# Kernel optimization log

Measured on AMD Instinct MI355X. Metric: run time of the kernel, lower is better.

The kernel has to match this reference:

```python
import jax, jax.numpy as jnp
import numpy as np

B, T, I, L, D, O = 256, 512, 512, 128, 4, 2
LN_EPS = 1e-5

def setup_inputs() -> dict:
    key = jax.random.key(0)
    ks = jax.random.split(key, 7)
    x = jax.random.normal(ks[0], (B, T, I), jnp.float32)
    # Xavier-ish scaling keeps the recurrence numerically tame
    W_in = jax.random.normal(ks[1], (L, D, I), jnp.float32) * (1.0 / np.sqrt(I))
    W_liquid = jax.random.normal(ks[2], (L, D, L), jnp.float32) * (1.0 / np.sqrt(L))
    W_gate = jax.random.normal(ks[3], (L, D), jnp.float32)
    b_liquid = jnp.zeros((L,), jnp.float32)
    W_out = jax.random.normal(ks[4], (O, L), jnp.float32) * (1.0 / np.sqrt(L))
    b_out = jnp.zeros((O,), jnp.float32)
    ln_w = jnp.ones((L,), jnp.float32)
    ln_b = jnp.zeros((L,), jnp.float32)
    leaky_rate = jnp.asarray(0.3, jnp.float32)
    return {"x": x, "W_in": W_in, "W_liquid": W_liquid, "W_gate": W_gate,
            "b_liquid": b_liquid, "W_out": W_out, "b_out": b_out,
            "ln_w": ln_w, "ln_b": ln_b, "leaky_rate": leaky_rate}

def reference(x, W_in, W_liquid, W_gate, b_liquid, W_out, b_out, ln_w, ln_b, leaky_rate):
    # Liquid dendritic RNN. Dropout is identity (eval mode).
    gate = jax.nn.sigmoid(W_gate)                                   # [L,D]
    # Input branch has no recurrent dependency -> batch it over all timesteps
    in_br = jax.nn.relu(jnp.einsum('ldi,bti->btld', W_in, x))       # [B,T,L,D]
    merged_in = jnp.einsum('btld,ld->btl', in_br, gate)             # [B,T,L]
    alpha = jax.nn.sigmoid(leaky_rate)

    def step(state, m_in_t):                                        # state [B,L]
        rec_br = jax.nn.relu(jnp.einsum('ldh,bh->bld', W_liquid, state))
        merged_rec = jnp.einsum('bld,ld->bl', rec_br, gate)
        li = m_in_t + merged_rec + b_liquid                         # [B,L]
        mu = jnp.mean(li, axis=-1, keepdims=True)
        var = jnp.var(li, axis=-1, keepdims=True)
        li = (li - mu) * jax.lax.rsqrt(var + LN_EPS) * ln_w + ln_b
        new_state = (1.0 - alpha) * state + alpha * jnp.tanh(li)
        return new_state, None

    state0 = jnp.zeros((x.shape[0], W_in.shape[0]), x.dtype)
    final_state, _ = jax.lax.scan(step, state0, jnp.swapaxes(merged_in, 0, 1))
    return final_state @ W_out.T + b_out                            # [B,O]
```

## Files before the change

kernel.cpp:

```cpp
#include <hip/hip_runtime.h>
#include <hip/hip_bf16.h>
#include <stdint.h>


typedef __bf16 bf16x8 __attribute__((ext_vector_type(8)));
typedef float f32x4_t __attribute__((ext_vector_type(4)));

__device__ inline unsigned short f2bf(float f) {
    union { float f; unsigned u; } v; v.f = f;
    unsigned r = v.u + 0x7fffu + ((v.u >> 16) & 1u);
    return (unsigned short)(r >> 16);
}

__global__ __launch_bounds__(256, 2)
void gemm_in_kernel(const float* __restrict__ x, const float* __restrict__ W_in,
                    const float* __restrict__ W_gate, float* __restrict__ merged)
{
    __shared__ unsigned short As[128 * 32];
    __shared__ unsigned short Bs[128 * 32];

    const int tid = threadIdx.x;
    const int m0 = blockIdx.y * 128;
    const int n0 = blockIdx.x * 128;
    const int lane = tid & 63;
    const int wid  = tid >> 6;
    const int wr = wid >> 1, wc = wid & 1;
    const int fr = lane & 15, fq = lane >> 4;

    f32x4_t acc[4][4];
    #pragma unroll
    for (int i = 0; i < 4; ++i)
        #pragma unroll
        for (int j = 0; j < 4; ++j)
            acc[i][j] = (f32x4_t){0.f, 0.f, 0.f, 0.f};

    for (int k0 = 0; k0 < 512; k0 += 32) {
        #pragma unroll
        for (int p = 0; p < 4; ++p) {
            int ch = tid + p * 256;
            int r  = ch >> 3;
            int c  = ch & 7;
            float4 va = *(const float4*)(x    + (size_t)(m0 + r) * 512 + k0 + c * 4);
            float4 vb = *(const float4*)(W_in + (size_t)(n0 + r) * 512 + k0 + c * 4);
            ushort4 ha, hb;
            ha.x = f2bf(va.x); ha.y = f2bf(va.y); ha.z = f2bf(va.z); ha.w = f2bf(va.w);
            hb.x = f2bf(vb.x); hb.y = f2bf(vb.y); hb.z = f2bf(vb.z); hb.w = f2bf(vb.w);
            *(ushort4*)(&As[r * 32 + c * 4]) = ha;
            *(ushort4*)(&Bs[r * 32 + c * 4]) = hb;
        }
        __syncthreads();

        bf16x8 af[4], bfr[4];
        #pragma unroll
        for (int mi = 0; mi < 4; ++mi)
            af[mi] = *(const bf16x8*)(&As[(wr * 64 + mi * 16 + fr) * 32 + fq * 8]);
        #pragma unroll
        for (int ni = 0; ni < 4; ++ni)
            bfr[ni] = *(const bf16x8*)(&Bs[(wc * 64 + ni * 16 + fr) * 32 + fq * 8]);

        #pragma unroll
        for (int mi = 0; mi < 4; ++mi)
            #pragma unroll
            for (int ni = 0; ni < 4; ++ni)
                acc[mi][ni] = __builtin_amdgcn_mfma_f32_16x16x32_bf16(
                                  af[mi], bfr[ni], acc[mi][ni], 0, 0, 0);
        __syncthreads();
    }

    float gv[4];
    #pragma unroll
    for (int ni = 0; ni < 4; ++ni) {
        int n = n0 + wc * 64 + ni * 16 + fr;
        gv[ni] = 1.f / (1.f + __expf(-W_gate[n]));
    }
    #pragma unroll
    for (int mi = 0; mi < 4; ++mi) {
        #pragma unroll
        for (int ni = 0; ni < 4; ++ni) {
            int n = n0 + wc * 64 + ni * 16 + fr;
            int l = n >> 2;
            #pragma unroll
            for (int j = 0; j < 4; ++j) {
                float v = acc[mi][ni][j];
                float r = fmaxf(v, 0.f) * gv[ni];
                r += __shfl_xor(r, 1);
                r += __shfl_xor(r, 2);
                if ((lane & 3) == 0) {
                    int row = m0 + wr * 64 + mi * 16 + fq * 4 + j;
                    merged[(size_t)row * 128 + l] = r;
                }
            }
        }
    }
}

__global__ __launch_bounds__(512, 2)
void scan_kernel(const float* __restrict__ merged, const float* __restrict__ W_liq,
                 const float* __restrict__ W_gate, const float* __restrict__ b_liq,
                 const float* __restrict__ W_out, const float* __restrict__ b_out,
                 const float* __restrict__ ln_w, const float* __restrict__ ln_b,
                 const float* __restrict__ leaky, float* __restrict__ out)
{
    __shared__ __align__(16) unsigned short s_bf[128];
    __shared__ __align__(16) float red[16];
    __shared__ float s_final[128];

    const int tid  = threadIdx.x;
    const int b    = blockIdx.x;
    const int lane = tid & 63;
    const int w    = tid >> 6;
    const int fr   = lane & 15;
    const int fq   = lane >> 4;

    bf16x8 wfrag[4][4];
    #pragma unroll
    for (int mi = 0; mi < 4; ++mi) {
        const float* wrow = W_liq + (size_t)(w * 64 + mi * 16 + fr) * 128;
        #pragma unroll
        for (int kk = 0; kk < 4; ++kk) {
            float4 f0 = *(const float4*)(wrow + kk * 32 + fq * 8);
            float4 f1 = *(const float4*)(wrow + kk * 32 + fq * 8 + 4);
            union { unsigned short u[8]; bf16x8 v; } cv;
            cv.u[0] = f2bf(f0.x); cv.u[1] = f2bf(f0.y);
            cv.u[2] = f2bf(f0.z); cv.u[3] = f2bf(f0.w);
            cv.u[4] = f2bf(f1.x); cv.u[5] = f2bf(f1.y);
            cv.u[6] = f2bf(f1.z); cv.u[7] = f2bf(f1.w);
            wfrag[mi][kk] = cv.v;
        }
    }

    int   l_mi[4];
    float gv[4][4], blv[4], lwv[4], lbv[4];
    size_t midx[4];
    #pragma unroll
    for (int mi = 0; mi < 4; ++mi) {
        int l = w * 16 + mi * 4 + fq;
        l_mi[mi] = l;
        #pragma unroll
        for (int r = 0; r < 4; ++r)
            gv[mi][r] = 1.f / (1.f + __expf(-W_gate[l * 4 + r]));
        blv[mi] = b_liq[l];
        lwv[mi] = ln_w[l];
        lbv[mi] = ln_b[l];
        midx[mi] = (size_t)b * 65536 + l;
    }
    const float alpha = 1.f / (1.f + __expf(-leaky[0]));
    const float oma   = 1.f - alpha;

    float s_reg[4] = {0.f, 0.f, 0.f, 0.f};
    float cur[4];
    #pragma unroll
    for (int mi = 0; mi < 4; ++mi) cur[mi] = merged[midx[mi]];

    if (tid < 64) ((unsigned*)s_bf)[tid] = 0u;
    __syncthreads();

    const f32x4_t z = {0.f, 0.f, 0.f, 0.f};

    for (int t = 0; t < 512; ++t) {
        bf16x8 bfr[4];
        #pragma unroll
        for (int kk = 0; kk < 4; ++kk)
            bfr[kk] = *(const bf16x8*)(&s_bf[kk * 32 + fq * 8]);

        float nxt[4] = {0.f, 0.f, 0.f, 0.f};
        if (t < 511) {
            #pragma unroll
            for (int mi = 0; mi < 4; ++mi)
                nxt[mi] = merged[midx[mi] + (size_t)(t + 1) * 128];
        }

        f32x4_t acc[4];
        #pragma unroll
        for (int mi = 0; mi < 4; ++mi)
            acc[mi] = __builtin_amdgcn_mfma_f32_16x16x32_bf16(wfrag[mi][0], bfr[0], z, 0, 0, 0);
        #pragma unroll
        for (int kk = 1; kk < 4; ++kk)
            #pragma unroll
            for (int mi = 0; mi < 4; ++mi)
                acc[mi] = __builtin_amdgcn_mfma_f32_16x16x32_bf16(wfrag[mi][kk], bfr[kk], acc[mi], 0, 0, 0);

        float li[4], v1 = 0.f, v2 = 0.f;
        #pragma unroll
        for (int mi = 0; mi < 4; ++mi) {
            float mr = gv[mi][0] * fmaxf(acc[mi][0], 0.f);
            mr = fmaf(gv[mi][1], fmaxf(acc[mi][1], 0.f), mr);
            mr = fmaf(gv[mi][2], fmaxf(acc[mi][2], 0.f), mr);
            mr = fmaf(gv[mi][3], fmaxf(acc[mi][3], 0.f), mr);
            li[mi] = cur[mi] + mr + blv[mi];
            v1 += li[mi];
            v2 = fmaf(li[mi], li[mi], v2);
        }
        v1 += __shfl_xor(v1, 16);  v2 += __shfl_xor(v2, 16);
        v1 += __shfl_xor(v1, 32);  v2 += __shfl_xor(v2, 32);
        if (lane == 0) { red[w] = v1; red[8 + w] = v2; }
        __syncthreads();

        float4 ra = *(const float4*)&red[0], rb = *(const float4*)&red[4];
        float4 rc = *(const float4*)&red[8], rd = *(const float4*)&red[12];
        float S1 = ((ra.x + ra.y) + (ra.z + ra.w)) + ((rb.x + rb.y) + (rb.z + rb.w));
        float S2 = ((rc.x + rc.y) + (rc.z + rc.w)) + ((rd.x + rd.y) + (rd.z + rd.w));
        float mean = S1 * (1.f / 128.f);
        float var  = fmaf(-mean, mean, S2 * (1.f / 128.f));
        float rstd = rsqrtf(var + 1e-5f);

        #pragma unroll
        for (int mi = 0; mi < 4; ++mi) {
            float t1 = rstd * lwv[mi];
            float xn = fmaf(li[mi], t1, fmaf(-mean, t1, lbv[mi]));
            float e  = __expf(2.f * xn);
            float th = fmaf(-2.f, __builtin_amdgcn_rcpf(e + 1.f), 1.f);
            float ns = fmaf(oma, s_reg[mi], alpha * th);
            s_reg[mi] = ns;
            cur[mi]   = nxt[mi];
        }
        if (fr == 0) {
            #pragma unroll
            for (int mi = 0; mi < 4; ++mi)
                s_bf[l_mi[mi]] = f2bf(s_reg[mi]);
        }
        __syncthreads();
    }

    if (fr == 0) {
        #pragma unroll
        for (int mi = 0; mi < 4; ++mi) s_final[l_mi[mi]] = s_reg[mi];
    }
    __syncthreads();
    if (tid < 2) {
        float accO = b_out[tid];
        #pragma unroll
        for (int h = 0; h < 128; ++h)
            accO = fmaf(s_final[h], W_out[tid * 128 + h], accO);
        out[b * 2 + tid] = accO;
    }
}

extern "C" void kernel_launch(void* const* d_in, const int* in_sizes, int n_in,
                              void* d_out, int out_size, void* d_ws, size_t ws_size,
                              hipStream_t stream)
{
    const float* x      = (const float*)d_in[0];
    const float* W_in   = (const float*)d_in[1];
    const float* W_liq  = (const float*)d_in[2];
    const float* W_gate = (const float*)d_in[3];
    const float* b_liq  = (const float*)d_in[4];
    const float* W_out  = (const float*)d_in[5];
    const float* b_out  = (const float*)d_in[6];
    const float* ln_w   = (const float*)d_in[7];
    const float* ln_b   = (const float*)d_in[8];
    const float* leaky  = (const float*)d_in[9];
    float* out    = (float*)d_out;
    float* merged = (float*)d_ws;

    gemm_in_kernel<<<dim3(4, 1024), 256, 0, stream>>>(x, W_in, W_gate, merged);
    scan_kernel<<<256, 512, 0, stream>>>(merged, W_liq, W_gate, b_liq,
                                         W_out, b_out, ln_w, ln_b, leaky, out);
}
```

Measured before the change: 690.5 us.

## Transpose merged input to time-major, vectorize scan loads, split MFMA chains, lighter barriers

The GEMM kernel now writes the merged input as [B][L][T], so each scan thread can fetch four consecutive timesteps with one float4 load, double-buffered two chunks ahead. The scan loop is unrolled in groups of four steps, and the K=128 MFMA accumulation is split into two independent chains that are summed at the end, shortening the serial dependency. __syncthreads is replaced with an explicit lgkmcnt wait plus s_barrier. The trade-off is a strided, uncoalesced store pattern in the GEMM epilogue, and the hand-written barrier relies on the compiler not reordering global memory accesses around it.

```diff
diff --git a/kernel.cpp b/kernel.cpp
--- a/kernel.cpp
+++ b/kernel.cpp
@@ -12,9 +12,14 @@
     return (unsigned short)(r >> 16);
 }
 
+__device__ inline void lds_barrier() {
+    asm volatile("s_waitcnt lgkmcnt(0)" ::: "memory");
+    __builtin_amdgcn_s_barrier();
+}
+
 __global__ __launch_bounds__(256, 2)
 void gemm_in_kernel(const float* __restrict__ x, const float* __restrict__ W_in,
-                    const float* __restrict__ W_gate, float* __restrict__ merged)
+                    const float* __restrict__ W_gate, float* __restrict__ mt)
 {
     __shared__ unsigned short As[128 * 32];
     __shared__ unsigned short Bs[128 * 32];
@@ -87,7 +92,9 @@
                 r += __shfl_xor(r, 2);
                 if ((lane & 3) == 0) {
                     int row = m0 + wr * 64 + mi * 16 + fq * 4 + j;
-                    merged[(size_t)row * 128 + l] = r;
+                    int bb = row >> 9;
+                    int tt = row & 511;
+                    mt[(size_t)bb * 65536 + (size_t)l * 512 + tt] = r;
                 }
             }
         }
@@ -95,7 +102,7 @@
 }
 
 __global__ __launch_bounds__(512, 2)
-void scan_kernel(const float* __restrict__ merged, const float* __restrict__ W_liq,
+void scan_kernel(const float* __restrict__ mt, const float* __restrict__ W_liq,
                  const float* __restrict__ W_gate, const float* __restrict__ b_liq,
                  const float* __restrict__ W_out, const float* __restrict__ b_out,
                  const float* __restrict__ ln_w, const float* __restrict__ ln_b,
@@ -142,84 +149,98 @@
         blv[mi] = b_liq[l];
         lwv[mi] = ln_w[l];
         lbv[mi] = ln_b[l];
-        midx[mi] = (size_t)b * 65536 + l;
+        midx[mi] = (size_t)b * 65536 + (size_t)l * 512;
     }
     const float alpha = 1.f / (1.f + __expf(-leaky[0]));
     const float oma   = 1.f - alpha;
 
     float s_reg[4] = {0.f, 0.f, 0.f, 0.f};
-    float cur[4];
-    #pragma unroll
-    for (int mi = 0; mi < 4; ++mi) cur[mi] = merged[midx[mi]];
+
+    float4 cur4[4], nxt4[4];
+    #pragma unroll
+    for (int mi = 0; mi < 4; ++mi) cur4[mi] = *(const float4*)(mt + midx[mi]);
+    #pragma unroll
+    for (int mi = 0; mi < 4; ++mi) nxt4[mi] = *(const float4*)(mt + midx[mi] + 4);
 
     if (tid < 64) ((unsigned*)s_bf)[tid] = 0u;
-    __syncthreads();
+    lds_barrier();
 
     const f32x4_t z = {0.f, 0.f, 0.f, 0.f};
 
-    for (int t = 0; t < 512; ++t) {
-        bf16x8 bfr[4];
-        #pragma unroll
-        for (int kk = 0; kk < 4; ++kk)
-            bfr[kk] = *(const bf16x8*)(&s_bf[kk * 32 + fq * 8]);
-
-        float nxt[4] = {0.f, 0.f, 0.f, 0.f};
-        if (t < 511) {
+    for (int ts = 0; ts < 512; ts += 4) {
+        float4 ld4[4];
+        if (ts < 504) {
             #pragma unroll
             for (int mi = 0; mi < 4; ++mi)
-                nxt[mi] = merged[midx[mi] + (size_t)(t + 1) * 128];
-        }
-
-        f32x4_t acc[4];
-        #pragma unroll
-        for (int mi = 0; mi < 4; ++mi)
-            acc[mi] = __builtin_amdgcn_mfma_f32_16x16x32_bf16(wfrag[mi][0], bfr[0], z, 0, 0, 0);
-        #pragma unroll
-        for (int kk = 1; kk < 4; ++kk)
-            #pragma unroll
-            for (int mi = 0; mi < 4; ++mi)
-                acc[mi] = __builtin_amdgcn_mfma_f32_16x16x32_bf16(wfrag[mi][kk], bfr[kk], acc[mi], 0, 0, 0);
-
-        float li[4], v1 = 0.f, v2 = 0.f;
-        #pragma unroll
-        for (int mi = 0; mi < 4; ++mi) {
-            float mr = gv[mi][0] * fmaxf(acc[mi][0], 0.f);
-            mr = fmaf(gv[mi][1], fmaxf(acc[mi][1], 0.f), mr);
-            mr = fmaf(gv[mi][2], fmaxf(acc[mi][2], 0.f), mr);
-            mr = fmaf(gv[mi][3], fmaxf(acc[mi][3], 0.f), mr);
-            li[mi] = cur[mi] + mr + blv[mi];
-            v1 += li[mi];
-            v2 = fmaf(li[mi], li[mi], v2);
-        }
-        v1 += __shfl_xor(v1, 16);  v2 += __shfl_xor(v2, 16);
-        v1 += __shfl_xor(v1, 32);  v2 += __shfl_xor(v2, 32);
-        if (lane == 0) { red[w] = v1; red[8 + w] = v2; }
-        __syncthreads();
-
-        float4 ra = *(const float4*)&red[0], rb = *(const float4*)&red[4];
-        float4 rc = *(const float4*)&red[8], rd = *(const float4*)&red[12];
-        float S1 = ((ra.x + ra.y) + (ra.z + ra.w)) + ((rb.x + rb.y) + (rb.z + rb.w));
-        float S2 = ((rc.x + rc.y) + (rc.z + rc.w)) + ((rd.x + rd.y) + (rd.z + rd.w));
-        float mean = S1 * (1.f / 128.f);
-        float var  = fmaf(-mean, mean, S2 * (1.f / 128.f));
-        float rstd = rsqrtf(var + 1e-5f);
-
-        #pragma unroll
-        for (int mi = 0; mi < 4; ++mi) {
-            float t1 = rstd * lwv[mi];
-            float xn = fmaf(li[mi], t1, fmaf(-mean, t1, lbv[mi]));
-            float e  = __expf(2.f * xn);
-            float th = fmaf(-2.f, __builtin_amdgcn_rcpf(e + 1.f), 1.f);
-            float ns = fmaf(oma, s_reg[mi], alpha * th);
-            s_reg[mi] = ns;
-            cur[mi]   = nxt[mi];
-        }
-        if (fr == 0) {
-            #pragma unroll
-            for (int mi = 0; mi < 4; ++mi)
-                s_bf[l_mi[mi]] = f2bf(s_reg[mi]);
-        }
-        __syncthreads();
+                ld4[mi] = *(const float4*)(mt + midx[mi] + ts + 8);
+        }
+
+        #pragma unroll
+        for (int ph = 0; ph < 4; ++ph) {
+            bf16x8 bfr[4];
+            #pragma unroll
+            for (int kk = 0; kk < 4; ++kk)
+                bfr[kk] = *(const bf16x8*)(&s_bf[kk * 32 + fq * 8]);
+
+            f32x4_t a0[4], a1[4];
+            #pragma unroll
+            for (int mi = 0; mi < 4; ++mi) {
+                a0[mi] = __builtin_amdgcn_mfma_f32_16x16x32_bf16(wfrag[mi][0], bfr[0], z, 0, 0, 0);
+                a1[mi] = __builtin_amdgcn_mfma_f32_16x16x32_bf16(wfrag[mi][2], bfr[2], z, 0, 0, 0);
+            }
+            #pragma unroll
+            for (int mi = 0; mi < 4; ++mi) {
+                a0[mi] = __builtin_amdgcn_mfma_f32_16x16x32_bf16(wfrag[mi][1], bfr[1], a0[mi], 0, 0, 0);
+                a1[mi] = __builtin_amdgcn_mfma_f32_16x16x32_bf16(wfrag[mi][3], bfr[3], a1[mi], 0, 0, 0);
+            }
+
+            float li[4], v1 = 0.f, v2 = 0.f;
+            #pragma unroll
+            for (int mi = 0; mi < 4; ++mi) {
+                f32x4_t s4 = a0[mi] + a1[mi];
+                float mr = gv[mi][0] * fmaxf(s4[0], 0.f);
+                mr = fmaf(gv[mi][1], fmaxf(s4[1], 0.f), mr);
+                mr = fmaf(gv[mi][2], fmaxf(s4[2], 0.f), mr);
+                mr = fmaf(gv[mi][3], fmaxf(s4[3], 0.f), mr);
+                li[mi] = cur4[mi][ph] + mr + blv[mi];
+                v1 += li[mi];
+                v2 = fmaf(li[mi], li[mi], v2);
+            }
+            v1 += __shfl_xor(v1, 16);  v2 += __shfl_xor(v2, 16);
+            v1 += __shfl_xor(v1, 32);  v2 += __shfl_xor(v2, 32);
+            if (lane == 0) { red[w] = v1; red[8 + w] = v2; }
+            lds_barrier();
+
+            float4 ra = *(const float4*)&red[0], rb = *(const float4*)&red[4];
+            float4 rc = *(const float4*)&red[8], rd = *(const float4*)&red[12];
+            float S1 = ((ra.x + ra.y) + (ra.z + ra.w)) + ((rb.x + rb.y) + (rb.z + rb.w));
+            float S2 = ((rc.x + rc.y) + (rc.z + rc.w)) + ((rd.x + rd.y) + (rd.z + rd.w));
+            float mean = S1 * (1.f / 128.f);
+            float var  = fmaf(-mean, mean, S2 * (1.f / 128.f));
+            float rstd = rsqrtf(var + 1e-5f);
+
+            #pragma unroll
+            for (int mi = 0; mi < 4; ++mi) {
+                float t1 = rstd * lwv[mi];
+                float xn = fmaf(li[mi], t1, fmaf(-mean, t1, lbv[mi]));
+                float e  = __expf(2.f * xn);
+                float th = fmaf(-2.f, __builtin_amdgcn_rcpf(e + 1.f), 1.f);
+                s_reg[mi] = fmaf(oma, s_reg[mi], alpha * th);
+            }
+            if (fr == 0) {
+                #pragma unroll
+                for (int mi = 0; mi < 4; ++mi)
+                    s_bf[l_mi[mi]] = f2bf(s_reg[mi]);
+            }
+            lds_barrier();
+        }
+
+        #pragma unroll
+        for (int mi = 0; mi < 4; ++mi) cur4[mi] = nxt4[mi];
+        if (ts < 504) {
+            #pragma unroll
+            for (int mi = 0; mi < 4; ++mi) nxt4[mi] = ld4[mi];
+        }
     }
 
     if (fr == 0) {
@@ -250,10 +271,10 @@
     const float* ln_w   = (const float*)d_in[7];
     const float* ln_b   = (const float*)d_in[8];
     const float* leaky  = (const float*)d_in[9];
-    float* out    = (float*)d_out;
-    float* merged = (float*)d_ws;
-
-    gemm_in_kernel<<<dim3(4, 1024), 256, 0, stream>>>(x, W_in, W_gate, merged);
-    scan_kernel<<<256, 512, 0, stream>>>(merged, W_liq, W_gate, b_liq,
+    float* out = (float*)d_out;
+    float* mt  = (float*)d_ws;
+
+    gemm_in_kernel<<<dim3(4, 1024), 256, 0, stream>>>(x, W_in, W_gate, mt);
+    scan_kernel<<<256, 512, 0, stream>>>(mt, W_liq, W_gate, b_liq,
                                          W_out, b_out, ln_w, ln_b, leaky, out);
 }
```

After: 703.5 us. About the same (+1.9%).
